# Kernel optimization log

Measured on AMD Instinct MI355X. Metric: run time of the kernel, lower is better.

Reference implementation:

```python
import jax, jax.numpy as jnp
import numpy as np

H, DH, C = 16, 64, 1024  # num_head, head_size, embed_size
B, T = 4, 2048

def setup_inputs() -> dict:
    key = jax.random.key(0)
    ks = jax.random.split(key, 6)
    s = 1.0 / np.sqrt(C)
    x  = jax.random.normal(ks[0], (B, T, C), dtype=jnp.float32)
    # per-head projection weights, stacked: [H, C, DH] (PyTorch Linear computes x @ W.T; we store W.T directly)
    Wq = jax.random.uniform(ks[1], (H, C, DH), dtype=jnp.float32, minval=-s, maxval=s)
    Wk = jax.random.uniform(ks[2], (H, C, DH), dtype=jnp.float32, minval=-s, maxval=s)
    Wv = jax.random.uniform(ks[3], (H, C, DH), dtype=jnp.float32, minval=-s, maxval=s)
    Wo = jax.random.uniform(ks[4], (C, C), dtype=jnp.float32, minval=-s, maxval=s)
    bo = jax.random.uniform(ks[5], (C,), dtype=jnp.float32, minval=-s, maxval=s)
    return {"x": x, "Wq": Wq, "Wk": Wk, "Wv": Wv, "Wo": Wo, "bo": bo}

def reference(x, Wq, Wk, Wv, Wo, bo):
    # Dropout layers act as identity (eval mode).
    q = jnp.einsum('btc,hcd->bhtd', x, Wq)
    k = jnp.einsum('btc,hcd->bhtd', x, Wk)
    v = jnp.einsum('btc,hcd->bhtd', x, Wv)
    scale = 1.0 / np.sqrt(DH).astype(np.float32)
    wei = jnp.einsum('bhtd,bhsd->bhts', q, k) * scale  # [B,H,T,T]
    Tn = x.shape[1]
    causal = jnp.tril(jnp.ones((Tn, Tn), dtype=bool))
    wei = jnp.where(causal, wei, -jnp.inf)
    wei = jax.nn.softmax(wei, axis=-1)
    out = jnp.einsum('bhts,bhsd->bhtd', wei, v)  # [B,H,T,DH]
    out = out.transpose(0, 2, 1, 3).reshape(x.shape[0], Tn, H * DH)  # concat heads
    return out @ Wo + bo
```

## Files before the change

kernel.cpp:

```cpp
#include <hip/hip_runtime.h>
#include <hip/hip_bf16.h>

typedef __attribute__((ext_vector_type(8))) short short8;
typedef __attribute__((ext_vector_type(4))) short s4v;
typedef __attribute__((ext_vector_type(4))) float floatx4;

static constexpr int Hn = 16, DHn = 64, Cn = 1024;
static constexpr int Bn = 4, Tn = 2048;
static constexpr int Mtot = Bn * Tn;
static constexpr size_t QKV_STRIDE = (size_t)Bn * Hn * Tn * DHn;

__device__ __forceinline__ unsigned short bfbits(float f) {
    __hip_bfloat16 h = __float2bfloat16(f);
    return __builtin_bit_cast(unsigned short, h);
}

__device__ __forceinline__ void gl_lds16(const void* g, void* lds_base) {
    __builtin_amdgcn_global_load_lds(
        (const __attribute__((address_space(1))) unsigned int*)g,
        (__attribute__((address_space(3))) unsigned int*)lds_base, 16, 0, 0);
}

__global__ void conv_kernel(const float4* __restrict__ src, ushort4* __restrict__ dst, int n4) {
    int i = blockIdx.x * blockDim.x + threadIdx.x;
    if (i < n4) {
        float4 v = src[i];
        ushort4 o;
        o.x = bfbits(v.x); o.y = bfbits(v.y); o.z = bfbits(v.z); o.w = bfbits(v.w);
        dst[i] = o;
    }
}

__global__ void tconv_kernel(const float* __restrict__ src, __hip_bfloat16* __restrict__ dst,
                             int R, int C, float scale) {
    __shared__ float tile[32][33];
    const float* s = src + (size_t)blockIdx.z * R * C;
    __hip_bfloat16* d = dst + (size_t)blockIdx.z * R * C;
    int c0 = blockIdx.x * 32;
    int r0 = blockIdx.y * 32;
    int tx = threadIdx.x;
    int ty = threadIdx.y;
    for (int i = 0; i < 4; ++i) {
        int r = r0 + ty + i * 8;
        tile[ty + i * 8][tx] = s[(size_t)r * C + c0 + tx];
    }
    __syncthreads();
    for (int i = 0; i < 4; ++i) {
        int c = c0 + ty + i * 8;
        d[(size_t)c * R + r0 + tx] = __float2bfloat16(tile[tx][ty + i * 8] * scale);
    }
}

template<int MODE>
__global__ __launch_bounds__(256) void gemm_kernel(
    const __hip_bfloat16* __restrict__ A,
    const __hip_bfloat16* __restrict__ BT,
    const float* __restrict__ bias,
    __hip_bfloat16* __restrict__ out_qkv,
    float* __restrict__ out_f32)
{
    constexpr int K = Cn;
    constexpr int NSTEP = K / 64;
    __shared__ char smem[65536];

    const int m0 = blockIdx.x * 128;
    const int n0 = blockIdx.y * 128;

    const int tid = threadIdx.x;
    const int lane = tid & 63, wid = tid >> 6;
    const int wy = wid >> 1, wx = wid & 1;
    const int fr = lane & 15, g = lane >> 4;
    const int rxor = (fr & 7) << 4;

    floatx4 acc[4][4] = {};

    int srow[4], scol[4], doff[4];
#pragma unroll
    for (int i = 0; i < 4; ++i) {
        int byteoff = wid * 4096 + i * 1024 + lane * 16;
        int r = byteoff >> 7;
        int ch = (byteoff >> 4) & 7;
        srow[i] = r;
        scol[i] = (ch ^ (r & 7)) << 3;
        doff[i] = wid * 4096 + i * 1024;
    }

#pragma unroll
    for (int i = 0; i < 4; ++i) {
        gl_lds16(&A[(size_t)(m0 + srow[i]) * K + scol[i]], smem + doff[i]);
        gl_lds16(&BT[(size_t)(n0 + srow[i]) * K + scol[i]], smem + 16384 + doff[i]);
    }
    asm volatile("s_waitcnt vmcnt(0)" ::: "memory");
    asm volatile("s_barrier" ::: "memory");

    int cur = 0;
    for (int t = 0; t < NSTEP; ++t) {
        if (t + 1 < NSTEP) {
            const int k0 = (t + 1) * 64;
            char* dst = smem + (cur ^ 1) * 32768;
#pragma unroll
            for (int i = 0; i < 4; ++i) {
                gl_lds16(&A[(size_t)(m0 + srow[i]) * K + k0 + scol[i]], dst + doff[i]);
                gl_lds16(&BT[(size_t)(n0 + srow[i]) * K + k0 + scol[i]], dst + 16384 + doff[i]);
            }
        }
        const char* lA0 = smem + cur * 32768;
        const char* lB0 = lA0 + 16384;
#pragma unroll
        for (int kk = 0; kk < 2; ++kk) {
            short8 af[4], bf[4];
#pragma unroll
            for (int t4 = 0; t4 < 4; ++t4) {
                af[t4] = *(const short8*)(lA0 + (wy * 64 + t4 * 16 + fr) * 128 + ((kk * 64 + g * 16) ^ rxor));
                bf[t4] = *(const short8*)(lB0 + (wx * 64 + t4 * 16 + fr) * 128 + ((kk * 64 + g * 16) ^ rxor));
            }
            __builtin_amdgcn_s_setprio(1);
#pragma unroll
            for (int tm = 0; tm < 4; ++tm)
#pragma unroll
                for (int tn = 0; tn < 4; ++tn)
                    acc[tm][tn] = __builtin_amdgcn_mfma_f32_16x16x32_bf16(af[tm], bf[tn], acc[tm][tn], 0, 0, 0);
            __builtin_amdgcn_s_setprio(0);
        }
        asm volatile("s_waitcnt vmcnt(0)" ::: "memory");
        asm volatile("s_barrier" ::: "memory");
        cur ^= 1;
    }

    for (int tm = 0; tm < 4; ++tm) {
        int rbase = m0 + wy * 64 + tm * 16 + g * 4;
        for (int tn = 0; tn < 4; ++tn) {
            int nc = n0 + wx * 64 + tn * 16 + fr;
            if (MODE == 0) {
                int w = nc >> 10, rem = nc & 1023, hh = rem >> 6, dd = rem & 63;
                if (w == 2) {
                    int b = rbase >> 11, t0 = rbase & 2047;
                    ushort4 pk;
                    pk.x = bfbits(acc[tm][tn][0]);
                    pk.y = bfbits(acc[tm][tn][1]);
                    pk.z = bfbits(acc[tm][tn][2]);
                    pk.w = bfbits(acc[tm][tn][3]);
                    *(ushort4*)(&out_qkv[2 * QKV_STRIDE +
                        ((size_t)((b * Hn + hh) * DHn + dd)) * Tn + t0]) = pk;
                } else {
                    for (int r = 0; r < 4; ++r) {
                        int m = rbase + r;
                        int b = m >> 11, t = m & 2047;
                        out_qkv[(size_t)w * QKV_STRIDE + (((size_t)(b * Hn + hh) * Tn + t) << 6) + dd] =
                            __float2bfloat16(acc[tm][tn][r]);
                    }
                }
            } else {
                float bs = bias[nc];
                for (int r = 0; r < 4; ++r) {
                    int m = rbase + r;
                    out_f32[(size_t)m * Cn + nc] = acc[tm][tn][r] + bs;
                }
            }
        }
    }
}

__global__ __launch_bounds__(256) void attn_kernel(
    const __hip_bfloat16* __restrict__ q,
    const __hip_bfloat16* __restrict__ k,
    const __hip_bfloat16* __restrict__ vt,
    __hip_bfloat16* __restrict__ ao)
{
    __shared__ char smem[49152];

    const int id = blockIdx.x;
    const int xcd = id & 7;
    const int rnk = id >> 3;
    const int tile = 15 - (rnk >> 3);
    const int bh = xcd * 8 + (rnk & 7);
    const int b = bh >> 4, h = bh & 15;
    const int tid = threadIdx.x, lane = tid & 63, wid = tid >> 6;
    const int fr = lane & 15, g = lane >> 4;
    const size_t base = (size_t)bh * Tn * DHn;
    const int rxor = (fr & 7) << 4;

    const int r0 = wid * 16 + (lane >> 3);
    const int c8 = ((lane & 7) ^ (r0 & 7)) * 8;
    const int ldk0 = wid * 2048;

    short8 ones;
#pragma unroll
    for (int z = 0; z < 8; ++z) ones[z] = (short)0x3F80;

    const int qb0 = tile * 128;
    const int q0 = qb0 + wid * 32;
    const int nkv = qb0 / 64 + 2;

    short8 aq[2][2];
#pragma unroll
    for (int rq = 0; rq < 2; ++rq)
#pragma unroll
        for (int kk = 0; kk < 2; ++kk)
            aq[rq][kk] = *(const short8*)(&q[base + (size_t)(q0 + rq * 16 + fr) * DHn + kk * 32 + g * 8]);

    floatx4 o[2][4] = {};
    floatx4 o5[2] = {};

#pragma unroll
    for (int jj = 0; jj < 2; ++jj) {
        char* kd = smem + jj * 8192 + ldk0;
        char* vd = smem + 24576 + jj * 8192 + ldk0;
        const int v0 = jj * 64;
        gl_lds16(&k[base + (size_t)(v0 + r0) * DHn + c8], kd);
        gl_lds16(&k[base + (size_t)(v0 + r0 + 8) * DHn + c8], kd + 1024);
        gl_lds16(&vt[base + (size_t)r0 * Tn + v0 + c8], vd);
        gl_lds16(&vt[base + (size_t)(r0 + 8) * Tn + v0 + c8], vd + 1024);
    }
    asm volatile("s_waitcnt vmcnt(4)" ::: "memory");
    __builtin_amdgcn_s_barrier();

    int bufc = 0;
    for (int j = 0; j < nkv; ++j) {
        const int kv0 = j * 64;

        if (kv0 < q0 + 32) {
            const char* lkc = smem + bufc * 8192;
            const char* lvc = smem + 24576 + bufc * 8192;

            floatx4 s[2][4] = {};
            __builtin_amdgcn_s_setprio(1);
#pragma unroll
            for (int kk = 0; kk < 2; ++kk)
#pragma unroll
                for (int cg = 0; cg < 4; ++cg) {
                    short8 kf = *(const short8*)(lkc + (cg * 16 + fr) * 128 + ((g * 16 + kk * 64) ^ rxor));
                    s[0][cg] = __builtin_amdgcn_mfma_f32_16x16x32_bf16(kf, aq[0][kk], s[0][cg], 0, 0, 0);
                    s[1][cg] = __builtin_amdgcn_mfma_f32_16x16x32_bf16(kf, aq[1][kk], s[1][cg], 0, 0, 0);
                }
            __builtin_amdgcn_s_setprio(0);

            if (kv0 + 64 > q0) {
#pragma unroll
                for (int rq = 0; rq < 2; ++rq) {
                    int qg = q0 + rq * 16 + fr;
#pragma unroll
                    for (int cg = 0; cg < 4; ++cg) {
                        int kg = kv0 + cg * 16 + g * 4;
#pragma unroll
                        for (int r = 0; r < 4; ++r)
                            if (kg + r > qg) s[rq][cg][r] = -1e30f;
                    }
                }
            }

            short8 pb[2][2];
#pragma unroll
            for (int rq = 0; rq < 2; ++rq) {
#pragma unroll
                for (int cg = 0; cg < 4; ++cg)
#pragma unroll
                    for (int r = 0; r < 4; ++r)
                        s[rq][cg][r] = __builtin_amdgcn_exp2f(s[rq][cg][r]);
#pragma unroll
                for (int kt = 0; kt < 2; ++kt) {
                    short8 pk;
#pragma unroll
                    for (int r = 0; r < 4; ++r) {
                        pk[r]     = (short)bfbits(s[rq][2 * kt][r]);
                        pk[r + 4] = (short)bfbits(s[rq][2 * kt + 1][r]);
                    }
                    pb[rq][kt] = pk;
                }
            }

            __builtin_amdgcn_s_setprio(1);
#pragma unroll
            for (int rq = 0; rq < 2; ++rq)
#pragma unroll
                for (int kt = 0; kt < 2; ++kt)
                    o5[rq] = __builtin_amdgcn_mfma_f32_16x16x32_bf16(ones, pb[rq][kt], o5[rq], 0, 0, 0);
#pragma unroll
            for (int kt = 0; kt < 2; ++kt)
#pragma unroll
                for (int dg = 0; dg < 4; ++dg) {
                    const int vrow = (dg * 16 + fr) * 128;
                    s4v lo = *(const s4v*)(lvc + vrow + ((kt * 64 + 8 * g) ^ rxor));
                    s4v hi = *(const s4v*)(lvc + vrow + ((kt * 64 + 32 + 8 * g) ^ rxor));
                    short8 vf = __builtin_shufflevector(lo, hi, 0, 1, 2, 3, 4, 5, 6, 7);
                    o[0][dg] = __builtin_amdgcn_mfma_f32_16x16x32_bf16(vf, pb[0][kt], o[0][dg], 0, 0, 0);
                    o[1][dg] = __builtin_amdgcn_mfma_f32_16x16x32_bf16(vf, pb[1][kt], o[1][dg], 0, 0, 0);
                }
            __builtin_amdgcn_s_setprio(0);
        }

        {
            int bi = bufc + 2; if (bi >= 3) bi -= 3;
            const int nv0 = kv0 + 128;
            char* kd = smem + bi * 8192 + ldk0;
            char* vd = smem + 24576 + bi * 8192 + ldk0;
            gl_lds16(&k[base + (size_t)(nv0 + r0) * DHn + c8], kd);
            gl_lds16(&k[base + (size_t)(nv0 + r0 + 8) * DHn + c8], kd + 1024);
            gl_lds16(&vt[base + (size_t)r0 * Tn + nv0 + c8], vd);
            gl_lds16(&vt[base + (size_t)(r0 + 8) * Tn + nv0 + c8], vd + 1024);
        }
        asm volatile("s_waitcnt vmcnt(4)" ::: "memory");
        __builtin_amdgcn_s_barrier();
        bufc = (bufc == 2) ? 0 : bufc + 1;
    }

    asm volatile("s_waitcnt vmcnt(0)" ::: "memory");
    __syncthreads();

    char* myscr = smem + wid * 4096;
    const int rr = lane >> 2, cc = lane & 3;
#pragma unroll
    for (int rq = 0; rq < 2; ++rq) {
        const float inv = 1.0f / o5[rq][0];
#pragma unroll
        for (int dg = 0; dg < 4; ++dg) {
            floatx4 wv = o[rq][dg] * inv;
            *(floatx4*)(myscr + fr * 256 + ((dg * 64 + g * 16) ^ rxor)) = wv;
        }
        asm volatile("s_waitcnt lgkmcnt(0)" ::: "memory");
        float4 f0 = *(const float4*)(myscr + rr * 256 + ((cc * 64 + 0) ^ ((rr & 7) << 4)));
        float4 f1 = *(const float4*)(myscr + rr * 256 + ((cc * 64 + 16) ^ ((rr & 7) << 4)));
        float4 f2 = *(const float4*)(myscr + rr * 256 + ((cc * 64 + 32) ^ ((rr & 7) << 4)));
        float4 f3 = *(const float4*)(myscr + rr * 256 + ((cc * 64 + 48) ^ ((rr & 7) << 4)));
        short8 pk0, pk1;
        pk0[0] = (short)bfbits(f0.x); pk0[1] = (short)bfbits(f0.y);
        pk0[2] = (short)bfbits(f0.z); pk0[3] = (short)bfbits(f0.w);
        pk0[4] = (short)bfbits(f1.x); pk0[5] = (short)bfbits(f1.y);
        pk0[6] = (short)bfbits(f1.z); pk0[7] = (short)bfbits(f1.w);
        pk1[0] = (short)bfbits(f2.x); pk1[1] = (short)bfbits(f2.y);
        pk1[2] = (short)bfbits(f2.z); pk1[3] = (short)bfbits(f2.w);
        pk1[4] = (short)bfbits(f3.x); pk1[5] = (short)bfbits(f3.y);
        pk1[6] = (short)bfbits(f3.z); pk1[7] = (short)bfbits(f3.w);
        size_t orow = ((size_t)(b * Tn + q0 + rq * 16 + rr)) * Cn + h * 64 + cc * 16;
        *(short8*)(&ao[orow]) = pk0;
        *(short8*)(&ao[orow + 8]) = pk1;
        asm volatile("s_waitcnt lgkmcnt(0)" ::: "memory");
    }
}

extern "C" void kernel_launch(void* const* d_in, const int* in_sizes, int n_in,
                              void* d_out, int out_size, void* d_ws, size_t ws_size,
                              hipStream_t stream) {
    const float* x  = (const float*)d_in[0];
    const float* Wq = (const float*)d_in[1];
    const float* Wk = (const float*)d_in[2];
    const float* Wv = (const float*)d_in[3];
    const float* Wo = (const float*)d_in[4];
    const float* bo = (const float*)d_in[5];
    float* out = (float*)d_out;

    char* ws = (char*)d_ws;
    __hip_bfloat16* xb  = (__hip_bfloat16*)(ws);
    __hip_bfloat16* wT  = (__hip_bfloat16*)(ws + 16777216);
    __hip_bfloat16* woT = (__hip_bfloat16*)(ws + 23068672);
    __hip_bfloat16* qb  = (__hip_bfloat16*)(ws + 25165824);
    __hip_bfloat16* ao  = (__hip_bfloat16*)(ws + 75497472);

    conv_kernel<<<(Mtot * Cn / 4 + 255) / 256, 256, 0, stream>>>(
        (const float4*)x, (ushort4*)xb, Mtot * Cn / 4);
    tconv_kernel<<<dim3(2, 32, 16), dim3(32, 8), 0, stream>>>(Wq, wT + 0 * 1048576, Cn, DHn, 0.125f * 1.44269504088896f);
    tconv_kernel<<<dim3(2, 32, 16), dim3(32, 8), 0, stream>>>(Wk, wT + 1 * 1048576, Cn, DHn, 1.0f);
    tconv_kernel<<<dim3(2, 32, 16), dim3(32, 8), 0, stream>>>(Wv, wT + 2 * 1048576, Cn, DHn, 1.0f);
    tconv_kernel<<<dim3(32, 32, 1), dim3(32, 8), 0, stream>>>(Wo, woT, Cn, Cn, 1.0f);

    gemm_kernel<0><<<dim3(Mtot / 128, 3072 / 128), 256, 0, stream>>>(
        xb, wT, nullptr, qb, nullptr);

    attn_kernel<<<dim3(1024), 256, 0, stream>>>(
        qb, qb + QKV_STRIDE, qb + 2 * QKV_STRIDE, ao);

    gemm_kernel<1><<<dim3(Mtot / 128, Cn / 128), 256, 0, stream>>>(
        ao, woT, bo, nullptr, out);
}
```

Measured before the change: 156.1 us.

## Use 256x256 tile GEMM for QKV projection and packed bf16 conversion in attention

```diff
diff --git a/kernel.cpp b/kernel.cpp
--- a/kernel.cpp
+++ b/kernel.cpp
@@ -4,6 +4,7 @@
 typedef __attribute__((ext_vector_type(8))) short short8;
 typedef __attribute__((ext_vector_type(4))) short s4v;
 typedef __attribute__((ext_vector_type(4))) float floatx4;
+typedef __attribute__((ext_vector_type(4))) unsigned int u32x4;
 
 static constexpr int Hn = 16, DHn = 64, Cn = 1024;
 static constexpr int Bn = 4, Tn = 2048;
@@ -13,6 +14,12 @@
 __device__ __forceinline__ unsigned short bfbits(float f) {
     __hip_bfloat16 h = __float2bfloat16(f);
     return __builtin_bit_cast(unsigned short, h);
+}
+
+__device__ __forceinline__ unsigned int cvtpk(float a, float b) {
+    unsigned int r;
+    asm("v_cvt_pk_bf16_f32 %0, %1, %2" : "=v"(r) : "v"(a), "v"(b));
+    return r;
 }
 
 __device__ __forceinline__ void gl_lds16(const void* g, void* lds_base) {
@@ -51,12 +58,105 @@
     }
 }
 
-template<int MODE>
+__global__ __launch_bounds__(512, 2) void gemm256_kernel(
+    const __hip_bfloat16* __restrict__ A,
+    const __hip_bfloat16* __restrict__ BT,
+    __hip_bfloat16* __restrict__ out_qkv)
+{
+    constexpr int K = Cn;
+    constexpr int NSTEP = K / 64;
+    __shared__ char smem[131072];
+
+    const int m0 = blockIdx.x * 256;
+    const int n0 = blockIdx.y * 256;
+    const int tid = threadIdx.x;
+    const int lane = tid & 63, wid = tid >> 6;
+    const int wm = wid >> 2, wn = wid & 3;
+    const int fr = lane & 15, g = lane >> 4;
+    const int rxor = (fr & 7) << 4;
+
+    floatx4 acc[8][4] = {};
+
+    const int lrow = lane >> 3;
+    const int c8 = ((lane & 7) ^ (lrow & 7)) * 8;
+    const int wdst = wid * 1024;
+
+#pragma unroll
+    for (int i = 0; i < 4; ++i) {
+        int row = i * 64 + wid * 8 + lrow;
+        gl_lds16(&A[(size_t)(m0 + row) * K + c8], smem + i * 8192 + wdst);
+        gl_lds16(&BT[(size_t)(n0 + row) * K + c8], smem + 32768 + i * 8192 + wdst);
+    }
+    asm volatile("s_waitcnt vmcnt(0)" ::: "memory");
+    asm volatile("s_barrier" ::: "memory");
+
+    int cur = 0;
+    for (int t = 0; t < NSTEP; ++t) {
+        if (t + 1 < NSTEP) {
+            const int k0 = (t + 1) * 64;
+            char* dst = smem + (cur ^ 1) * 65536;
+#pragma unroll
+            for (int i = 0; i < 4; ++i) {
+                int row = i * 64 + wid * 8 + lrow;
+                gl_lds16(&A[(size_t)(m0 + row) * K + k0 + c8], dst + i * 8192 + wdst);
+                gl_lds16(&BT[(size_t)(n0 + row) * K + k0 + c8], dst + 32768 + i * 8192 + wdst);
+            }
+        }
+        const char* lA0 = smem + cur * 65536;
+        const char* lB0 = lA0 + 32768;
+#pragma unroll
+        for (int kk = 0; kk < 2; ++kk) {
+            short8 bf[4];
+#pragma unroll
+            for (int nf = 0; nf < 4; ++nf)
+                bf[nf] = *(const short8*)(lB0 + (wn * 64 + nf * 16 + fr) * 128 + ((kk * 64 + g * 16) ^ rxor));
+            __builtin_amdgcn_s_setprio(1);
+#pragma unroll
+            for (int mf = 0; mf < 8; ++mf) {
+                short8 af = *(const short8*)(lA0 + (wm * 128 + mf * 16 + fr) * 128 + ((kk * 64 + g * 16) ^ rxor));
+#pragma unroll
+                for (int nf = 0; nf < 4; ++nf)
+                    acc[mf][nf] = __builtin_amdgcn_mfma_f32_16x16x32_bf16(af, bf[nf], acc[mf][nf], 0, 0, 0);
+            }
+            __builtin_amdgcn_s_setprio(0);
+        }
+        asm volatile("s_waitcnt vmcnt(0)" ::: "memory");
+        asm volatile("s_barrier" ::: "memory");
+        cur ^= 1;
+    }
+
+#pragma unroll
+    for (int mf = 0; mf < 8; ++mf) {
+        int rbase = m0 + wm * 128 + mf * 16 + g * 4;
+#pragma unroll
+        for (int nf = 0; nf < 4; ++nf) {
+            int nc = n0 + wn * 64 + nf * 16 + fr;
+            int w = nc >> 10, rem = nc & 1023, hh = rem >> 6, dd = rem & 63;
+            if (w == 2) {
+                int b = rbase >> 11, t0 = rbase & 2047;
+                ushort4 pk;
+                pk.x = bfbits(acc[mf][nf][0]);
+                pk.y = bfbits(acc[mf][nf][1]);
+                pk.z = bfbits(acc[mf][nf][2]);
+                pk.w = bfbits(acc[mf][nf][3]);
+                *(ushort4*)(&out_qkv[2 * QKV_STRIDE +
+                    ((size_t)((b * Hn + hh) * DHn + dd)) * Tn + t0]) = pk;
+            } else {
+                for (int r = 0; r < 4; ++r) {
+                    int m = rbase + r;
+                    int b = m >> 11, tq = m & 2047;
+                    out_qkv[(size_t)w * QKV_STRIDE + (((size_t)(b * Hn + hh) * Tn + tq) << 6) + dd] =
+                        __float2bfloat16(acc[mf][nf][r]);
+                }
+            }
+        }
+    }
+}
+
 __global__ __launch_bounds__(256) void gemm_kernel(
     const __hip_bfloat16* __restrict__ A,
     const __hip_bfloat16* __restrict__ BT,
     const float* __restrict__ bias,
-    __hip_bfloat16* __restrict__ out_qkv,
     float* __restrict__ out_f32)
 {
     constexpr int K = Cn;
@@ -131,31 +231,10 @@
         int rbase = m0 + wy * 64 + tm * 16 + g * 4;
         for (int tn = 0; tn < 4; ++tn) {
             int nc = n0 + wx * 64 + tn * 16 + fr;
-            if (MODE == 0) {
-                int w = nc >> 10, rem = nc & 1023, hh = rem >> 6, dd = rem & 63;
-                if (w == 2) {
-                    int b = rbase >> 11, t0 = rbase & 2047;
-                    ushort4 pk;
-                    pk.x = bfbits(acc[tm][tn][0]);
-                    pk.y = bfbits(acc[tm][tn][1]);
-                    pk.z = bfbits(acc[tm][tn][2]);
-                    pk.w = bfbits(acc[tm][tn][3]);
-                    *(ushort4*)(&out_qkv[2 * QKV_STRIDE +
-                        ((size_t)((b * Hn + hh) * DHn + dd)) * Tn + t0]) = pk;
-                } else {
-                    for (int r = 0; r < 4; ++r) {
-                        int m = rbase + r;
-                        int b = m >> 11, t = m & 2047;
-                        out_qkv[(size_t)w * QKV_STRIDE + (((size_t)(b * Hn + hh) * Tn + t) << 6) + dd] =
-                            __float2bfloat16(acc[tm][tn][r]);
-                    }
-                }
-            } else {
-                float bs = bias[nc];
-                for (int r = 0; r < 4; ++r) {
-                    int m = rbase + r;
-                    out_f32[(size_t)m * Cn + nc] = acc[tm][tn][r] + bs;
-                }
+            float bs = bias[nc];
+            for (int r = 0; r < 4; ++r) {
+                int m = rbase + r;
+                out_f32[(size_t)m * Cn + nc] = acc[tm][tn][r] + bs;
             }
         }
     }
@@ -259,13 +338,12 @@
                         s[rq][cg][r] = __builtin_amdgcn_exp2f(s[rq][cg][r]);
 #pragma unroll
                 for (int kt = 0; kt < 2; ++kt) {
-                    short8 pk;
-#pragma unroll
-                    for (int r = 0; r < 4; ++r) {
-                        pk[r]     = (short)bfbits(s[rq][2 * kt][r]);
-                        pk[r + 4] = (short)bfbits(s[rq][2 * kt + 1][r]);
-                    }
-                    pb[rq][kt] = pk;
+                    u32x4 wv;
+                    wv[0] = cvtpk(s[rq][2 * kt][0],     s[rq][2 * kt][1]);
+                    wv[1] = cvtpk(s[rq][2 * kt][2],     s[rq][2 * kt][3]);
+                    wv[2] = cvtpk(s[rq][2 * kt + 1][0], s[rq][2 * kt + 1][1]);
+                    wv[3] = cvtpk(s[rq][2 * kt + 1][2], s[rq][2 * kt + 1][3]);
+                    pb[rq][kt] = __builtin_bit_cast(short8, wv);
                 }
             }
 
@@ -363,12 +441,12 @@
     tconv_kernel<<<dim3(2, 32, 16), dim3(32, 8), 0, stream>>>(Wv, wT + 2 * 1048576, Cn, DHn, 1.0f);
     tconv_kernel<<<dim3(32, 32, 1), dim3(32, 8), 0, stream>>>(Wo, woT, Cn, Cn, 1.0f);
 
-    gemm_kernel<0><<<dim3(Mtot / 128, 3072 / 128), 256, 0, stream>>>(
-        xb, wT, nullptr, qb, nullptr);
+    gemm256_kernel<<<dim3(Mtot / 256, 3072 / 256), 512, 0, stream>>>(
+        xb, wT, qb);
 
     attn_kernel<<<dim3(1024), 256, 0, stream>>>(
         qb, qb + QKV_STRIDE, qb + 2 * QKV_STRIDE, ao);
 
-    gemm_kernel<1><<<dim3(Mtot / 128, Cn / 128), 256, 0, stream>>>(
-        ao, woT, bo, nullptr, out);
-}
+    gemm_kernel<<<dim3(Mtot / 128, Cn / 128), 256, 0, stream>>>(
+        ao, woT, bo, out);
+}
```

New measurement: 165.0 us. +5.7%, slower.

## Switch attention KV pipeline to double buffering and pack bf16 conversions

Applied to the files above, without the earlier changes.

```diff
diff --git a/kernel.cpp b/kernel.cpp
--- a/kernel.cpp
+++ b/kernel.cpp
@@ -4,6 +4,7 @@
 typedef __attribute__((ext_vector_type(8))) short short8;
 typedef __attribute__((ext_vector_type(4))) short s4v;
 typedef __attribute__((ext_vector_type(4))) float floatx4;
+typedef __attribute__((ext_vector_type(4))) unsigned int u32x4;
 
 static constexpr int Hn = 16, DHn = 64, Cn = 1024;
 static constexpr int Bn = 4, Tn = 2048;
@@ -13,6 +14,12 @@
 __device__ __forceinline__ unsigned short bfbits(float f) {
     __hip_bfloat16 h = __float2bfloat16(f);
     return __builtin_bit_cast(unsigned short, h);
+}
+
+__device__ __forceinline__ unsigned int cvtpk(float a, float b) {
+    unsigned int r;
+    asm("v_cvt_pk_bf16_f32 %0, %1, %2" : "=v"(r) : "v"(a), "v"(b));
+    return r;
 }
 
 __device__ __forceinline__ void gl_lds16(const void* g, void* lds_base) {
@@ -161,13 +168,13 @@
     }
 }
 
-__global__ __launch_bounds__(256) void attn_kernel(
+__global__ __launch_bounds__(256, 5) void attn_kernel(
     const __hip_bfloat16* __restrict__ q,
     const __hip_bfloat16* __restrict__ k,
     const __hip_bfloat16* __restrict__ vt,
     __hip_bfloat16* __restrict__ ao)
 {
-    __shared__ char smem[49152];
+    __shared__ char smem[32768];
 
     const int id = blockIdx.x;
     const int xcd = id & 7;
@@ -202,26 +209,34 @@
     floatx4 o[2][4] = {};
     floatx4 o5[2] = {};
 
-#pragma unroll
-    for (int jj = 0; jj < 2; ++jj) {
-        char* kd = smem + jj * 8192 + ldk0;
-        char* vd = smem + 24576 + jj * 8192 + ldk0;
-        const int v0 = jj * 64;
-        gl_lds16(&k[base + (size_t)(v0 + r0) * DHn + c8], kd);
-        gl_lds16(&k[base + (size_t)(v0 + r0 + 8) * DHn + c8], kd + 1024);
-        gl_lds16(&vt[base + (size_t)r0 * Tn + v0 + c8], vd);
-        gl_lds16(&vt[base + (size_t)(r0 + 8) * Tn + v0 + c8], vd + 1024);
-    }
-    asm volatile("s_waitcnt vmcnt(4)" ::: "memory");
+    {
+        char* kd = smem + ldk0;
+        char* vd = smem + 16384 + ldk0;
+        gl_lds16(&k[base + (size_t)r0 * DHn + c8], kd);
+        gl_lds16(&k[base + (size_t)(r0 + 8) * DHn + c8], kd + 1024);
+        gl_lds16(&vt[base + (size_t)r0 * Tn + c8], vd);
+        gl_lds16(&vt[base + (size_t)(r0 + 8) * Tn + c8], vd + 1024);
+    }
+    asm volatile("s_waitcnt vmcnt(0)" ::: "memory");
     __builtin_amdgcn_s_barrier();
 
-    int bufc = 0;
+    int cur = 0;
     for (int j = 0; j < nkv; ++j) {
         const int kv0 = j * 64;
 
+        {
+            const int nv0 = kv0 + 64;
+            char* kd = smem + (cur ^ 1) * 8192 + ldk0;
+            char* vd = smem + 16384 + (cur ^ 1) * 8192 + ldk0;
+            gl_lds16(&k[base + (size_t)(nv0 + r0) * DHn + c8], kd);
+            gl_lds16(&k[base + (size_t)(nv0 + r0 + 8) * DHn + c8], kd + 1024);
+            gl_lds16(&vt[base + (size_t)r0 * Tn + nv0 + c8], vd);
+            gl_lds16(&vt[base + (size_t)(r0 + 8) * Tn + nv0 + c8], vd + 1024);
+        }
+
         if (kv0 < q0 + 32) {
-            const char* lkc = smem + bufc * 8192;
-            const char* lvc = smem + 24576 + bufc * 8192;
+            const char* lkc = smem + cur * 8192;
+            const char* lvc = smem + 16384 + cur * 8192;
 
             floatx4 s[2][4] = {};
             __builtin_amdgcn_s_setprio(1);
@@ -259,13 +274,12 @@
                         s[rq][cg][r] = __builtin_amdgcn_exp2f(s[rq][cg][r]);
 #pragma unroll
                 for (int kt = 0; kt < 2; ++kt) {
-                    short8 pk;
-#pragma unroll
-                    for (int r = 0; r < 4; ++r) {
-                        pk[r]     = (short)bfbits(s[rq][2 * kt][r]);
-                        pk[r + 4] = (short)bfbits(s[rq][2 * kt + 1][r]);
-                    }
-                    pb[rq][kt] = pk;
+                    u32x4 wv;
+                    wv[0] = cvtpk(s[rq][2 * kt][0],     s[rq][2 * kt][1]);
+                    wv[1] = cvtpk(s[rq][2 * kt][2],     s[rq][2 * kt][3]);
+                    wv[2] = cvtpk(s[rq][2 * kt + 1][0], s[rq][2 * kt + 1][1]);
+                    wv[3] = cvtpk(s[rq][2 * kt + 1][2], s[rq][2 * kt + 1][3]);
+                    pb[rq][kt] = __builtin_bit_cast(short8, wv);
                 }
             }
 
@@ -289,23 +303,10 @@
             __builtin_amdgcn_s_setprio(0);
         }
 
-        {
-            int bi = bufc + 2; if (bi >= 3) bi -= 3;
-            const int nv0 = kv0 + 128;
-            char* kd = smem + bi * 8192 + ldk0;
-            char* vd = smem + 24576 + bi * 8192 + ldk0;
-            gl_lds16(&k[base + (size_t)(nv0 + r0) * DHn + c8], kd);
-            gl_lds16(&k[base + (size_t)(nv0 + r0 + 8) * DHn + c8], kd + 1024);
-            gl_lds16(&vt[base + (size_t)r0 * Tn + nv0 + c8], vd);
-            gl_lds16(&vt[base + (size_t)(r0 + 8) * Tn + nv0 + c8], vd + 1024);
-        }
-        asm volatile("s_waitcnt vmcnt(4)" ::: "memory");
+        asm volatile("s_waitcnt vmcnt(0)" ::: "memory");
         __builtin_amdgcn_s_barrier();
-        bufc = (bufc == 2) ? 0 : bufc + 1;
-    }
-
-    asm volatile("s_waitcnt vmcnt(0)" ::: "memory");
-    __syncthreads();
+        cur ^= 1;
+    }
 
     char* myscr = smem + wid * 4096;
     const int rr = lane >> 2, cc = lane & 3;
```

After: 220.1 us. +41.0%, slower.
